# Kernel tuning notes

Hardware: AMD Instinct MI355X
Metric: run time of the kernel (lower is better)

## Reference

```python
import jax, jax.numpy as jnp
import numpy as np

B, N, K, H, NHEADS, NIN = 4, 2000, 30, 128, 4, 256
DFF = 4 * H
EPS = 1e-6


def layer_norm(x, gain, bias):
    # torch .var() defaults to unbiased (ddof=1); denominator is (sigma + eps)
    mu = x.mean(-1, keepdims=True)
    sigma = jnp.sqrt(x.var(-1, ddof=1, keepdims=True) + EPS)
    return gain * (x - mu) / (sigma + EPS) + bias


def setup_inputs() -> dict:
    key = jax.random.key(0)
    ks = jax.random.split(key, 10)
    s = 0.05
    h_v = jax.random.normal(ks[0], (B, N, H), jnp.float32)
    h_e = jax.random.normal(ks[1], (B, N, K, NIN), jnp.float32)
    mask_attend = (jax.random.uniform(ks[2], (B, N, K)) < 0.9).astype(jnp.float32)
    mask_attend = mask_attend.at[..., 0].set(1.0)  # avoid all-masked rows -> NaN softmax
    mask_v = (jax.random.uniform(ks[3], (B, N)) < 0.95).astype(jnp.float32)
    return {
        "h_v": h_v,
        "h_e": h_e,
        "mask_v": mask_v,
        "mask_attend": mask_attend,
        "W_Q": jax.random.normal(ks[4], (H, H), jnp.float32) * s,
        "W_K": jax.random.normal(ks[5], (H, NIN), jnp.float32) * s,
        "W_V": jax.random.normal(ks[6], (H, NIN), jnp.float32) * s,
        "W_O": jax.random.normal(ks[7], (H, H), jnp.float32) * s,
        "gain0": jnp.ones((H,), jnp.float32),
        "bias0": jnp.zeros((H,), jnp.float32),
        "gain1": jnp.ones((H,), jnp.float32),
        "bias1": jnp.zeros((H,), jnp.float32),
        "W_in": jax.random.normal(ks[8], (DFF, H), jnp.float32) * s,
        "b_in": jnp.zeros((DFF,), jnp.float32),
        "W_out": jax.random.normal(ks[9], (H, DFF), jnp.float32) * s,
        "b_out": jnp.zeros((H,), jnp.float32),
    }


def reference(h_v, h_e, mask_v, mask_attend, W_Q, W_K, W_V, W_O,
              gain0, bias0, gain1, bias1, W_in, b_in, W_out, b_out):
    d = H // NHEADS
    # Neighbor attention (dropout is identity at inference)
    Q = (h_v @ W_Q.T).reshape(B, N, NHEADS, d)          # [B,N,h,d]
    Kp = (h_e @ W_K.T).reshape(B, N, K, NHEADS, d)      # [B,N,K,h,d]
    Vp = (h_e @ W_V.T).reshape(B, N, K, NHEADS, d)      # [B,N,K,h,d]
    logits = jnp.einsum('bnhd,bnkhd->bnhk', Q, Kp) / np.sqrt(d)
    mask = mask_attend[:, :, None, :]                   # [B,N,1,K] broadcast over heads
    neg_inf = jnp.finfo(logits.dtype).min
    attend = jax.nn.softmax(jnp.where(mask > 0, logits, neg_inf), axis=-1) * mask
    h_upd = jnp.einsum('bnhk,bnkhd->bnhd', attend, Vp).reshape(B, N, H)
    dh = h_upd @ W_O.T
    h = layer_norm(h_v + dh, gain0, bias0)
    # Position-wise FFN
    dh = jax.nn.relu(h @ W_in.T + b_in) @ W_out.T + b_out
    h = layer_norm(h + dh, gain1, bias1)
    return mask_v[..., None] * h
```

## Files before the change

### kernel.cpp

```cpp
#include <hip/hip_runtime.h>
#include <math.h>

#define TK 30
#define TH 128
#define TNIN 256
#define TDFF 512
#define NTOK 8000
#define ROWP 264

typedef __attribute__((ext_vector_type(8))) short short8v;
typedef __attribute__((ext_vector_type(4))) short short4v;
typedef __attribute__((ext_vector_type(4))) float f32x4;

constexpr float LN_EPS = 1e-6f;
constexpr float NEG_INF = -3.402823466e38f;
constexpr float INV_SQRT_D = 0.17677669529663687f;

static __device__ __forceinline__ unsigned short f2bf(float f) {
  unsigned u = __float_as_uint(f);
  u = u + 0x7fffu + ((u >> 16) & 1u);
  return (unsigned short)(u >> 16);
}
static __device__ __forceinline__ float bf2f(unsigned short s) {
  return __uint_as_float(((unsigned)s) << 16);
}
static __device__ __forceinline__ void gload16(const void* gsrc, void* ldst) {
  __builtin_amdgcn_global_load_lds(
      (const __attribute__((address_space(1))) unsigned int*)gsrc,
      (__attribute__((address_space(3))) unsigned int*)ldst, 16, 0, 0);
}

__global__ void conv_weights_kernel(const float* __restrict__ W_K,
                                    const float* __restrict__ W_V,
                                    const float* __restrict__ W_Q,
                                    const float* __restrict__ W_O,
                                    const float* __restrict__ W_in,
                                    const float* __restrict__ W_out,
                                    unsigned short* __restrict__ Wc2,
                                    unsigned short* __restrict__ Wq2,
                                    unsigned short* __restrict__ Wp2,
                                    unsigned short* __restrict__ Wi2,
                                    unsigned short* __restrict__ Wo2)
{
  int idx = blockIdx.x * 256 + threadIdx.x;
  if (idx < 65536) {
    int e = idx >> 3, j = idx & 7;
    int kk = e >> 10, n = (e >> 6) & 15, lane = e & 63;
    int r = n*16 + (lane & 15);
    int c = kk*32 + (lane >> 4)*8 + j;
    float v = (r < TH) ? W_K[(size_t)r*TNIN + c] : W_V[(size_t)(r-TH)*TNIN + c];
    Wc2[idx] = f2bf(v);
  } else if (idx < 81920) {
    int i2 = idx - 65536;
    int e = i2 >> 3, j = i2 & 7;
    int kk = e >> 9, n = (e >> 6) & 7, lane = e & 63;
    int r = n*16 + (lane & 15);
    int c = kk*32 + (lane >> 4)*8 + j;
    Wq2[i2] = f2bf(W_Q[(size_t)r*TH + c]);
  } else if (idx < 98304) {
    int ip = idx - 81920;
    int e = ip >> 3, j = ip & 7;
    int kk = e >> 9, n = (e >> 6) & 7, lane = e & 63;
    int r = n*16 + (lane & 15);
    int c = kk*32 + (lane >> 4)*8 + j;
    Wp2[ip] = f2bf(W_O[(size_t)r*TH + c]);
  } else if (idx < 163840) {
    int i3 = idx - 98304;
    int e = i3 >> 3, j = i3 & 7;
    int ks = e >> 11, n = (e >> 6) & 31, lane = e & 63;
    int r = n*16 + (lane & 15);
    int c = ks*32 + (lane >> 4)*8 + j;
    Wi2[i3] = f2bf(W_in[(size_t)r*TH + c]);
  } else {
    int i4 = idx - 163840;
    int e = i4 >> 3, j = i4 & 7;
    int ks = e >> 9, n = (e >> 6) & 7, lane = e & 63;
    int r = n*16 + (lane & 15);
    int c = ks*32 + (lane >> 4)*8 + j;
    Wo2[i4] = f2bf(W_out[(size_t)r*TDFF + c]);
  }
}

__global__ __launch_bounds__(512, 4) void kvattn_kernel(
    const float* __restrict__ A, const unsigned short* __restrict__ Wc2,
    const unsigned short* __restrict__ Wq2, const float* __restrict__ h_v,
    const float* __restrict__ mask_attend, float* __restrict__ ul)
{
  const int tid  = threadIdx.x;
  const int wave = tid >> 6;
  const int lane = tid & 63;
  const int lm   = lane & 15;
  const int lgp  = lane >> 4;
  const int mh   = wave >> 2;
  const int nq   = wave & 3;
  const int bn0  = blockIdx.x * 4;

  __shared__ __align__(16) char smem[73728];
  unsigned short* Bl  = (unsigned short*)smem;
  unsigned short* Al  = (unsigned short*)(smem + 49152);
  unsigned short* KVs = (unsigned short*)smem;
  float* att = (float*)(smem + 67584);
  float* hvp = (float*)(smem + 69632);
  float* qvp = (float*)(smem + 71680);

  if (tid < 128) {
    int tok = tid >> 5, q = tid & 31;
    *(float4*)&hvp[tok*128 + q*4] = *(const float4*)&h_v[(size_t)(bn0 + tok)*TH + q*4];
  }

  const int rowa = tid >> 2, cga = tid & 3;
  const int rowc = (rowa > 119) ? 119 : rowa;
  const float* aptr = A + ((size_t)blockIdx.x*120 + rowc)*TNIN + cga*8;

  #define ISSUE_B(K)                                                             \
    { gload16(Wc2 + (size_t)(K)*8192 + tid*8,       &Bl[((K)%3)*8192 + tid*8]);  \
      gload16(Wc2 + (size_t)(K)*8192 + (tid+512)*8, &Bl[((K)%3)*8192 + (tid+512)*8]); }

  #define WRITE_A(K, S)                                                     \
    { short8v w;                                                            \
      w[0]=(short)f2bf(ra[S][0].x); w[1]=(short)f2bf(ra[S][0].y);           \
      w[2]=(short)f2bf(ra[S][0].z); w[3]=(short)f2bf(ra[S][0].w);           \
      w[4]=(short)f2bf(ra[S][1].x); w[5]=(short)f2bf(ra[S][1].y);           \
      w[6]=(short)f2bf(ra[S][1].z); w[7]=(short)f2bf(ra[S][1].w);           \
      *(short8v*)&Al[(((K)&1)*128 + rowa)*40 + cga*8] = w; }

  float4 ra[3][2];
  f32x4 acc[4][4] = {};

  ra[0][0] = *(const float4*)(aptr + 0);
  ra[0][1] = *(const float4*)(aptr + 4);
  ISSUE_B(0);
  ISSUE_B(1);
  ra[1][0] = *(const float4*)(aptr + 32);
  ra[1][1] = *(const float4*)(aptr + 36);
  ra[2][0] = *(const float4*)(aptr + 64);
  ra[2][1] = *(const float4*)(aptr + 68);
  WRITE_A(0, 0);

  #pragma unroll
  for (int k = 0; k < 8; ++k) {
    if (k == 7)      asm volatile("s_waitcnt vmcnt(0)" ::: "memory");
    else if (k == 6) asm volatile("s_waitcnt vmcnt(4)" ::: "memory");
    else             asm volatile("s_waitcnt vmcnt(6)" ::: "memory");
    __builtin_amdgcn_s_barrier();

    if (k < 6) ISSUE_B(k+2);
    if (k < 5) {
      ra[k%3][0] = *(const float4*)(aptr + (k+3)*32);
      ra[k%3][1] = *(const float4*)(aptr + (k+3)*32 + 4);
    }

    short8v af[4];
    #pragma unroll
    for (int m = 0; m < 4; ++m)
      af[m] = *(const short8v*)&Al[((k&1)*128 + mh*64 + m*16 + lm)*40 + lgp*8];

    __builtin_amdgcn_s_setprio(1);
    #pragma unroll
    for (int n = 0; n < 4; ++n) {
      short8v b = *(const short8v*)&Bl[(k%3)*8192 + ((nq*4 + n)*64 + lane)*8];
      #pragma unroll
      for (int m = 0; m < 4; ++m)
        acc[m][n] = __builtin_amdgcn_mfma_f32_16x16x32_bf16(b, af[m], acc[m][n], 0, 0, 0);
    }
    __builtin_amdgcn_s_setprio(0);

    if (k < 7) WRITE_A(k+1, (k+1)%3);
  }
  #undef ISSUE_B
  #undef WRITE_A

  __syncthreads();

  #pragma unroll
  for (int m = 0; m < 4; ++m) {
    int row = mh*64 + m*16 + lm;
    #pragma unroll
    for (int n = 0; n < 4; ++n) {
      int col = nq*64 + n*16 + lgp*4;
      short4v p;
      p[0]=(short)f2bf(acc[m][n][0]); p[1]=(short)f2bf(acc[m][n][1]);
      p[2]=(short)f2bf(acc[m][n][2]); p[3]=(short)f2bf(acc[m][n][3]);
      *(short4v*)&KVs[row*ROWP + col] = p;
    }
  }

  {
    f32x4 qacc = {};
    const int tokc = (lm < 4) ? lm : 3;
    #pragma unroll
    for (int ks = 0; ks < 4; ++ks) {
      short8v wq = *(const short8v*)(Wq2 + ((size_t)(ks*8 + wave)*64 + lane)*8);
      const float* hp = hvp + tokc*128 + ks*32 + lgp*8;
      float4 lo = *(const float4*)hp;
      float4 hi = *(const float4*)(hp + 4);
      short8v ha;
      ha[0]=(short)f2bf(lo.x); ha[1]=(short)f2bf(lo.y);
      ha[2]=(short)f2bf(lo.z); ha[3]=(short)f2bf(lo.w);
      ha[4]=(short)f2bf(hi.x); ha[5]=(short)f2bf(hi.y);
      ha[6]=(short)f2bf(hi.z); ha[7]=(short)f2bf(hi.w);
      qacc = __builtin_amdgcn_mfma_f32_16x16x32_bf16(wq, ha, qacc, 0, 0, 0);
    }
    if (lm < 4) *(f32x4*)&qvp[lm*128 + wave*16 + lgp*4] = qacc;
  }
  __syncthreads();

  {
    int tok = tid >> 7, h = (tid >> 5) & 3, k = tid & 31;
    int gtok = bn0 + tok;
    float s = 0.f;
    float ma = 0.f;
    if (k < TK) {
      const float* qp = &qvp[tok*128 + h*32];
      const unsigned short* kp = &KVs[(tok*TK + k)*ROWP + h*32];
      #pragma unroll
      for (int j = 0; j < 4; ++j) {
        short8v kf = *(const short8v*)(kp + j*8);
        float4 qa = *(const float4*)(qp + j*8);
        float4 qb = *(const float4*)(qp + j*8 + 4);
        s += qa.x*bf2f((unsigned short)kf[0]) + qa.y*bf2f((unsigned short)kf[1])
           + qa.z*bf2f((unsigned short)kf[2]) + qa.w*bf2f((unsigned short)kf[3])
           + qb.x*bf2f((unsigned short)kf[4]) + qb.y*bf2f((unsigned short)kf[5])
           + qb.z*bf2f((unsigned short)kf[6]) + qb.w*bf2f((unsigned short)kf[7]);
      }
      ma = mask_attend[(size_t)gtok*TK + k];
    }
    bool ok = (k < TK) && (ma > 0.f);
    float val = ok ? s * INV_SQRT_D : NEG_INF;
    float mm = val;
    #pragma unroll
    for (int d = 16; d >= 1; d >>= 1) mm = fmaxf(mm, __shfl_xor(mm, d, 32));
    float e = ok ? expf(val - mm) : 0.f;
    float ss = e;
    #pragma unroll
    for (int d = 16; d >= 1; d >>= 1) ss += __shfl_xor(ss, d, 32);
    att[(tok*4 + h)*32 + k] = e / ss;
  }
  __syncthreads();

  {
    int tok = tid >> 7, c = tid & 127;
    int gtok = bn0 + tok;
    const float* ar = &att[(tok*4 + (c >> 5))*32];
    const unsigned short* vb = &KVs[tok*TK*ROWP + TH + c];
    float u = 0.f;
    #pragma unroll
    for (int k = 0; k < TK; ++k)
      u += ar[k] * bf2f(vb[k*ROWP]);
    ul[(size_t)gtok*TH + c] = u;
  }
}

__global__ __launch_bounds__(256) void ffn_all_kernel(
    const float* __restrict__ ul, const unsigned short* __restrict__ Wp2,
    const float* __restrict__ h_v,
    const float* __restrict__ gain0, const float* __restrict__ bias0,
    const unsigned short* __restrict__ Wi2, const unsigned short* __restrict__ Wo2,
    const float* __restrict__ b_in, const float* __restrict__ b_out,
    const float* __restrict__ gain1, const float* __restrict__ bias1,
    const float* __restrict__ mask_v, float* __restrict__ out)
{
  const int tid  = threadIdx.x;
  const int tok0 = blockIdx.x * 32;
  const int wave = tid >> 6;
  const int lane = tid & 63;
  const int lm   = lane & 15;
  const int lgp  = lane >> 4;

  __shared__ __align__(16) char smem[143616];
  unsigned short* Wp  = (unsigned short*)smem;
  unsigned short* Wst = (unsigned short*)(smem + 32768);
  unsigned short* At  = (unsigned short*)(smem + 98304);
  unsigned short* Zs  = (unsigned short*)(smem + 107008);
  float* bin  = (float*)(smem + 140288);
  float* part = (float*)(smem + 142336);
  float* red  = (float*)(smem + 143360);

  for (int t = tid; t < 1024; t += 256) {
    int row = t >> 5, q = t & 31;
    float4 v = *(const float4*)&ul[(size_t)(tok0+row)*TH + q*4];
    short4v w;
    w[0]=(short)f2bf(v.x); w[1]=(short)f2bf(v.y);
    w[2]=(short)f2bf(v.z); w[3]=(short)f2bf(v.w);
    *(short4v*)&At[row*136 + q*4] = w;
  }
  if (tid < 128) *(float4*)&bin[tid*4] = *(const float4*)&b_in[tid*4];
  #pragma unroll
  for (int p = 0; p < 8; ++p)
    gload16(Wp2 + (size_t)(tid + p*256)*8, &Wp[(tid + p*256)*8]);
  #pragma unroll
  for (int p = 0; p < 8; ++p)
    gload16(Wi2 + (size_t)(tid + p*256)*8, &Wst[(tid + p*256)*8]);

  asm volatile("s_waitcnt vmcnt(8)" ::: "memory");
  __syncthreads();

  f32x4 acco[2][2] = {};
  #pragma unroll
  for (int ks = 0; ks < 4; ++ks) {
    short8v a0 = *(const short8v*)&At[lm*136      + ks*32 + lgp*8];
    short8v a1 = *(const short8v*)&At[(16+lm)*136 + ks*32 + lgp*8];
    #pragma unroll
    for (int n = 0; n < 2; ++n) {
      short8v b = *(const short8v*)&Wp[((size_t)(ks*8 + wave*2 + n)*64 + lane)*8];
      acco[0][n] = __builtin_amdgcn_mfma_f32_16x16x32_bf16(b, a0, acco[0][n], 0, 0, 0);
      acco[1][n] = __builtin_amdgcn_mfma_f32_16x16x32_bf16(b, a1, acco[1][n], 0, 0, 0);
    }
  }

  f32x4 hn[2][2];
  {
    f32x4 x[2][2];
    float s1r[2] = {0.f, 0.f}, s2r[2] = {0.f, 0.f};
    #pragma unroll
    for (int m = 0; m < 2; ++m) {
      int row = m*16 + lm;
      #pragma unroll
      for (int n = 0; n < 2; ++n) {
        int col = (wave*2 + n)*16 + lgp*4;
        float4 hv = *(const float4*)&h_v[(size_t)(tok0+row)*TH + col];
        x[m][n][0] = acco[m][n][0] + hv.x;
        x[m][n][1] = acco[m][n][1] + hv.y;
        x[m][n][2] = acco[m][n][2] + hv.z;
        x[m][n][3] = acco[m][n][3] + hv.w;
        #pragma unroll
        for (int r = 0; r < 4; ++r) {
          s1r[m] += x[m][n][r];
          s2r[m] += x[m][n][r]*x[m][n][r];
        }
      }
    }
    #pragma unroll
    for (int m = 0; m < 2; ++m) {
      s1r[m] += __shfl_xor(s1r[m], 16); s2r[m] += __shfl_xor(s2r[m], 16);
      s1r[m] += __shfl_xor(s1r[m], 32); s2r[m] += __shfl_xor(s2r[m], 32);
    }
    if (lgp == 0) {
      part[(lm*4      + wave)*2 + 0] = s1r[0];
      part[(lm*4      + wave)*2 + 1] = s2r[0];
      part[((16+lm)*4 + wave)*2 + 0] = s1r[1];
      part[((16+lm)*4 + wave)*2 + 1] = s2r[1];
    }
    __syncthreads();
    if (tid < 32) {
      float s1 = 0.f, s2 = 0.f;
      #pragma unroll
      for (int w = 0; w < 4; ++w) { s1 += part[(tid*4+w)*2]; s2 += part[(tid*4+w)*2+1]; }
      float mu  = s1*(1.f/128.f);
      float var = (s2 - 128.f*mu*mu)*(1.f/127.f);
      red[tid*2]   = mu;
      red[tid*2+1] = 1.f/(sqrtf(var+LN_EPS)+LN_EPS);
    }
    __syncthreads();
    #pragma unroll
    for (int m = 0; m < 2; ++m) {
      int row = m*16 + lm;
      float mu = red[row*2], inv = red[row*2+1];
      #pragma unroll
      for (int n = 0; n < 2; ++n) {
        int col = (wave*2 + n)*16 + lgp*4;
        float4 g = *(const float4*)&gain0[col];
        float4 b = *(const float4*)&bias0[col];
        hn[m][n][0] = g.x*(x[m][n][0]-mu)*inv + b.x;
        hn[m][n][1] = g.y*(x[m][n][1]-mu)*inv + b.y;
        hn[m][n][2] = g.z*(x[m][n][2]-mu)*inv + b.z;
        hn[m][n][3] = g.w*(x[m][n][3]-mu)*inv + b.w;
        short4v p;
        p[0]=(short)f2bf(hn[m][n][0]); p[1]=(short)f2bf(hn[m][n][1]);
        p[2]=(short)f2bf(hn[m][n][2]); p[3]=(short)f2bf(hn[m][n][3]);
        *(short4v*)&At[row*136 + col] = p;
      }
    }
  }

  f32x4 acc1[2][8] = {};
  #pragma unroll
  for (int ks = 0; ks < 4; ++ks) {
    asm volatile("s_waitcnt vmcnt(0)" ::: "memory");
    __builtin_amdgcn_s_barrier();
    if (ks < 3) {
      #pragma unroll
      for (int p = 0; p < 8; ++p)
        gload16(Wi2 + (size_t)(ks+1)*16384 + (tid + p*256)*8,
                &Wst[((ks+1)&1)*16384 + (tid + p*256)*8]);
    } else {
      #pragma unroll
      for (int p = 0; p < 4; ++p)
        gload16(Wo2 + (size_t)(tid + p*256)*8, &Wst[(tid + p*256)*8]);
    }

    short8v a0 = *(const short8v*)&At[lm*136      + ks*32 + lgp*8];
    short8v a1 = *(const short8v*)&At[(16+lm)*136 + ks*32 + lgp*8];
    #pragma unroll
    for (int n = 0; n < 8; ++n) {
      short8v b = *(const short8v*)&Wst[(ks&1)*16384 + ((wave*8 + n)*64 + lane)*8];
      acc1[0][n] = __builtin_amdgcn_mfma_f32_16x16x32_bf16(b, a0, acc1[0][n], 0, 0, 0);
      acc1[1][n] = __builtin_amdgcn_mfma_f32_16x16x32_bf16(b, a1, acc1[1][n], 0, 0, 0);
    }
  }

  #pragma unroll
  for (int m = 0; m < 2; ++m) {
    int row = m*16 + lm;
    #pragma unroll
    for (int n = 0; n < 8; ++n) {
      int col = (wave*8 + n)*16 + lgp*4;
      float4 bv = *(const float4*)&bin[col];
      short4v p;
      p[0]=(short)f2bf(fmaxf(acc1[m][n][0] + bv.x, 0.f));
      p[1]=(short)f2bf(fmaxf(acc1[m][n][1] + bv.y, 0.f));
      p[2]=(short)f2bf(fmaxf(acc1[m][n][2] + bv.z, 0.f));
      p[3]=(short)f2bf(fmaxf(acc1[m][n][3] + bv.w, 0.f));
      *(short4v*)&Zs[row*520 + col] = p;
    }
  }

  f32x4 acc2[2][2] = {};
  #pragma unroll
  for (int ks2 = 0; ks2 < 8; ++ks2) {
    asm volatile("s_waitcnt vmcnt(0)" ::: "memory");
    __builtin_amdgcn_s_barrier();
    if (ks2 < 7) {
      #pragma unroll
      for (int p = 0; p < 4; ++p)
        gload16(Wo2 + (size_t)(ks2+1)*8192 + (tid + p*256)*8,
                &Wst[((ks2+1)&1)*8192 + (tid + p*256)*8]);
    }

    #pragma unroll
    for (int s = 0; s < 2; ++s) {
      int ks = ks2*2 + s;
      short8v a0 = *(const short8v*)&Zs[lm*520      + ks*32 + lgp*8];
      short8v a1 = *(const short8v*)&Zs[(16+lm)*520 + ks*32 + lgp*8];
      #pragma unroll
      for (int n = 0; n < 2; ++n) {
        short8v b = *(const short8v*)&Wst[(ks2&1)*8192 + s*4096 + ((wave*2 + n)*64 + lane)*8];
        acc2[0][n] = __builtin_amdgcn_mfma_f32_16x16x32_bf16(b, a0, acc2[0][n], 0, 0, 0);
        acc2[1][n] = __builtin_amdgcn_mfma_f32_16x16x32_bf16(b, a1, acc2[1][n], 0, 0, 0);
      }
    }
  }

  {
    f32x4 x[2][2];
    float s1r[2] = {0.f, 0.f}, s2r[2] = {0.f, 0.f};
    #pragma unroll
    for (int m = 0; m < 2; ++m) {
      #pragma unroll
      for (int n = 0; n < 2; ++n) {
        int col = (wave*2 + n)*16 + lgp*4;
        float4 bo = *(const float4*)&b_out[col];
        x[m][n][0] = acc2[m][n][0] + bo.x + hn[m][n][0];
        x[m][n][1] = acc2[m][n][1] + bo.y + hn[m][n][1];
        x[m][n][2] = acc2[m][n][2] + bo.z + hn[m][n][2];
        x[m][n][3] = acc2[m][n][3] + bo.w + hn[m][n][3];
        #pragma unroll
        for (int r = 0; r < 4; ++r) {
          s1r[m] += x[m][n][r];
          s2r[m] += x[m][n][r]*x[m][n][r];
        }
      }
    }
    #pragma unroll
    for (int m = 0; m < 2; ++m) {
      s1r[m] += __shfl_xor(s1r[m], 16); s2r[m] += __shfl_xor(s2r[m], 16);
      s1r[m] += __shfl_xor(s1r[m], 32); s2r[m] += __shfl_xor(s2r[m], 32);
    }
    if (lgp == 0) {
      part[(lm*4      + wave)*2 + 0] = s1r[0];
      part[(lm*4      + wave)*2 + 1] = s2r[0];
      part[((16+lm)*4 + wave)*2 + 0] = s1r[1];
      part[((16+lm)*4 + wave)*2 + 1] = s2r[1];
    }
    __syncthreads();
    if (tid < 32) {
      float s1 = 0.f, s2 = 0.f;
      #pragma unroll
      for (int w = 0; w < 4; ++w) { s1 += part[(tid*4+w)*2]; s2 += part[(tid*4+w)*2+1]; }
      float mu  = s1*(1.f/128.f);
      float var = (s2 - 128.f*mu*mu)*(1.f/127.f);
      red[tid*2]   = mu;
      red[tid*2+1] = 1.f/(sqrtf(var+LN_EPS)+LN_EPS);
    }
    __syncthreads();
    #pragma unroll
    for (int m = 0; m < 2; ++m) {
      int row = m*16 + lm;
      float mu = red[row*2], inv = red[row*2+1];
      float mv = mask_v[tok0 + row];
      #pragma unroll
      for (int n = 0; n < 2; ++n) {
        int col = (wave*2 + n)*16 + lgp*4;
        float4 g = *(const float4*)&gain1[col];
        float4 b = *(const float4*)&bias1[col];
        float4 y;
        y.x = mv*(g.x*(x[m][n][0]-mu)*inv + b.x);
        y.y = mv*(g.y*(x[m][n][1]-mu)*inv + b.y);
        y.z = mv*(g.z*(x[m][n][2]-mu)*inv + b.z);
        y.w = mv*(g.w*(x[m][n][3]-mu)*inv + b.w);
        *(float4*)&out[(size_t)(tok0+row)*TH + col] = y;
      }
    }
  }
}

extern "C" void kernel_launch(void* const* d_in, const int* in_sizes, int n_in,
                              void* d_out, int out_size, void* d_ws, size_t ws_size,
                              hipStream_t stream)
{
  const float* h_v         = (const float*)d_in[0];
  const float* h_e         = (const float*)d_in[1];
  const float* mask_v      = (const float*)d_in[2];
  const float* mask_attend = (const float*)d_in[3];
  const float* W_Q   = (const float*)d_in[4];
  const float* W_K   = (const float*)d_in[5];
  const float* W_V   = (const float*)d_in[6];
  const float* W_O   = (const float*)d_in[7];
  const float* gain0 = (const float*)d_in[8];
  const float* bias0 = (const float*)d_in[9];
  const float* gain1 = (const float*)d_in[10];
  const float* bias1 = (const float*)d_in[11];
  const float* W_in  = (const float*)d_in[12];
  const float* b_in  = (const float*)d_in[13];
  const float* W_out = (const float*)d_in[14];
  const float* b_out = (const float*)d_in[15];

  float* out = (float*)d_out;
  char* ws = (char*)d_ws;
  unsigned short* Wc2 = (unsigned short*)ws;
  unsigned short* Wq2 = (unsigned short*)(ws + 131072);
  unsigned short* Wp2 = (unsigned short*)(ws + 163840);
  unsigned short* Wi2 = (unsigned short*)(ws + 196608);
  unsigned short* Wo2 = (unsigned short*)(ws + 327680);
  float* ul = (float*)(ws + 458752);

  conv_weights_kernel<<<896, 256, 0, stream>>>(W_K, W_V, W_Q, W_O, W_in, W_out,
                                               Wc2, Wq2, Wp2, Wi2, Wo2);
  kvattn_kernel<<<NTOK/4, 512, 0, stream>>>(h_e, Wc2, Wq2, h_v, mask_attend, ul);
  ffn_all_kernel<<<NTOK/32, 256, 0, stream>>>(ul, Wp2, h_v, gain0, bias0,
                                              Wi2, Wo2, b_in, b_out,
                                              gain1, bias1, mask_v, out);
}
```

Baseline: 79.89 us.

## Halve kvattn block to 256 threads with each wave covering all 128 rows

The fused K/V projection and attention kernel now runs with 4 waves per block instead of 8. Each wave computes all 128 A-rows (8 M-fragments) for its 64-column slice, so the B operand is reused across twice as many MFMAs and waves no longer split rows. Global loads, the Q projection, and the softmax and value passes are redistributed across the smaller block, with two passes where needed. The cost is more accumulator registers per thread (32 f32x4) and half the threads for latency hiding. Shared memory stays at 73728 bytes per block, which may limit how many blocks fit per CU.

```diff
diff --git a/kernel.cpp b/kernel.cpp
--- a/kernel.cpp
+++ b/kernel.cpp
@@ -81,18 +81,16 @@
   }
 }
 
-__global__ __launch_bounds__(512, 4) void kvattn_kernel(
+__global__ __launch_bounds__(256, 2) void kvattn_kernel(
     const float* __restrict__ A, const unsigned short* __restrict__ Wc2,
     const unsigned short* __restrict__ Wq2, const float* __restrict__ h_v,
     const float* __restrict__ mask_attend, float* __restrict__ ul)
 {
   const int tid  = threadIdx.x;
-  const int wave = tid >> 6;
+  const int nq   = tid >> 6;
   const int lane = tid & 63;
   const int lm   = lane & 15;
   const int lgp  = lane >> 4;
-  const int mh   = wave >> 2;
-  const int nq   = wave & 3;
   const int bn0  = blockIdx.x * 4;
 
   __shared__ __align__(16) char smem[73728];
@@ -108,59 +106,67 @@
     *(float4*)&hvp[tok*128 + q*4] = *(const float4*)&h_v[(size_t)(bn0 + tok)*TH + q*4];
   }
 
-  const int rowa = tid >> 2, cga = tid & 3;
+  const int rowa = tid >> 1, ha = tid & 1;
   const int rowc = (rowa > 119) ? 119 : rowa;
-  const float* aptr = A + ((size_t)blockIdx.x*120 + rowc)*TNIN + cga*8;
-
-  #define ISSUE_B(K)                                                             \
-    { gload16(Wc2 + (size_t)(K)*8192 + tid*8,       &Bl[((K)%3)*8192 + tid*8]);  \
-      gload16(Wc2 + (size_t)(K)*8192 + (tid+512)*8, &Bl[((K)%3)*8192 + (tid+512)*8]); }
+  const float* aptr = A + ((size_t)blockIdx.x*120 + rowc)*TNIN + ha*16;
+
+  #define ISSUE_B(K)                                                               \
+    { gload16(Wc2 + (size_t)(K)*8192 + (tid      )*8, &Bl[((K)%3)*8192 + (tid      )*8]); \
+      gload16(Wc2 + (size_t)(K)*8192 + (tid+ 256 )*8, &Bl[((K)%3)*8192 + (tid+ 256 )*8]); \
+      gload16(Wc2 + (size_t)(K)*8192 + (tid+ 512 )*8, &Bl[((K)%3)*8192 + (tid+ 512 )*8]); \
+      gload16(Wc2 + (size_t)(K)*8192 + (tid+ 768 )*8, &Bl[((K)%3)*8192 + (tid+ 768 )*8]); }
+
+  #define LOAD_RA(S, K)                                                     \
+    { ra[S][0] = *(const float4*)(aptr + (K)*32);                           \
+      ra[S][1] = *(const float4*)(aptr + (K)*32 + 4);                       \
+      ra[S][2] = *(const float4*)(aptr + (K)*32 + 8);                       \
+      ra[S][3] = *(const float4*)(aptr + (K)*32 + 12); }
 
   #define WRITE_A(K, S)                                                     \
-    { short8v w;                                                            \
-      w[0]=(short)f2bf(ra[S][0].x); w[1]=(short)f2bf(ra[S][0].y);           \
-      w[2]=(short)f2bf(ra[S][0].z); w[3]=(short)f2bf(ra[S][0].w);           \
-      w[4]=(short)f2bf(ra[S][1].x); w[5]=(short)f2bf(ra[S][1].y);           \
-      w[6]=(short)f2bf(ra[S][1].z); w[7]=(short)f2bf(ra[S][1].w);           \
-      *(short8v*)&Al[(((K)&1)*128 + rowa)*40 + cga*8] = w; }
-
-  float4 ra[3][2];
-  f32x4 acc[4][4] = {};
-
-  ra[0][0] = *(const float4*)(aptr + 0);
-  ra[0][1] = *(const float4*)(aptr + 4);
+    { short8v w0, w1;                                                       \
+      w0[0]=(short)f2bf(ra[S][0].x); w0[1]=(short)f2bf(ra[S][0].y);         \
+      w0[2]=(short)f2bf(ra[S][0].z); w0[3]=(short)f2bf(ra[S][0].w);         \
+      w0[4]=(short)f2bf(ra[S][1].x); w0[5]=(short)f2bf(ra[S][1].y);         \
+      w0[6]=(short)f2bf(ra[S][1].z); w0[7]=(short)f2bf(ra[S][1].w);         \
+      w1[0]=(short)f2bf(ra[S][2].x); w1[1]=(short)f2bf(ra[S][2].y);         \
+      w1[2]=(short)f2bf(ra[S][2].z); w1[3]=(short)f2bf(ra[S][2].w);         \
+      w1[4]=(short)f2bf(ra[S][3].x); w1[5]=(short)f2bf(ra[S][3].y);         \
+      w1[6]=(short)f2bf(ra[S][3].z); w1[7]=(short)f2bf(ra[S][3].w);         \
+      *(short8v*)&Al[(((K)&1)*128 + rowa)*40 + ha*16    ] = w0;             \
+      *(short8v*)&Al[(((K)&1)*128 + rowa)*40 + ha*16 + 8] = w1; }
+
+  float4 ra[3][4];
+  f32x4 acc[8][4] = {};
+
+  LOAD_RA(0, 0);
   ISSUE_B(0);
   ISSUE_B(1);
-  ra[1][0] = *(const float4*)(aptr + 32);
-  ra[1][1] = *(const float4*)(aptr + 36);
-  ra[2][0] = *(const float4*)(aptr + 64);
-  ra[2][1] = *(const float4*)(aptr + 68);
+  LOAD_RA(1, 1);
+  LOAD_RA(2, 2);
   WRITE_A(0, 0);
 
   #pragma unroll
   for (int k = 0; k < 8; ++k) {
-    if (k == 7)      asm volatile("s_waitcnt vmcnt(0)" ::: "memory");
-    else if (k == 6) asm volatile("s_waitcnt vmcnt(4)" ::: "memory");
-    else             asm volatile("s_waitcnt vmcnt(6)" ::: "memory");
+    if      (k == 0) asm volatile("s_waitcnt vmcnt(8)"  ::: "memory");
+    else if (k <= 5) asm volatile("s_waitcnt vmcnt(12)" ::: "memory");
+    else if (k == 6) asm volatile("s_waitcnt vmcnt(8)"  ::: "memory");
+    else             asm volatile("s_waitcnt vmcnt(0)"  ::: "memory");
     __builtin_amdgcn_s_barrier();
 
     if (k < 6) ISSUE_B(k+2);
-    if (k < 5) {
-      ra[k%3][0] = *(const float4*)(aptr + (k+3)*32);
-      ra[k%3][1] = *(const float4*)(aptr + (k+3)*32 + 4);
-    }
-
-    short8v af[4];
-    #pragma unroll
-    for (int m = 0; m < 4; ++m)
-      af[m] = *(const short8v*)&Al[((k&1)*128 + mh*64 + m*16 + lm)*40 + lgp*8];
+    if (k < 5) LOAD_RA(k%3, k+3);
+
+    short8v af[8];
+    #pragma unroll
+    for (int m = 0; m < 8; ++m)
+      af[m] = *(const short8v*)&Al[((k&1)*128 + m*16 + lm)*40 + lgp*8];
 
     __builtin_amdgcn_s_setprio(1);
     #pragma unroll
     for (int n = 0; n < 4; ++n) {
       short8v b = *(const short8v*)&Bl[(k%3)*8192 + ((nq*4 + n)*64 + lane)*8];
       #pragma unroll
-      for (int m = 0; m < 4; ++m)
+      for (int m = 0; m < 8; ++m)
         acc[m][n] = __builtin_amdgcn_mfma_f32_16x16x32_bf16(b, af[m], acc[m][n], 0, 0, 0);
     }
     __builtin_amdgcn_s_setprio(0);
@@ -168,16 +174,17 @@
     if (k < 7) WRITE_A(k+1, (k+1)%3);
   }
   #undef ISSUE_B
+  #undef LOAD_RA
   #undef WRITE_A
 
   __syncthreads();
 
   #pragma unroll
-  for (int m = 0; m < 4; ++m) {
-    int row = mh*64 + m*16 + lm;
+  for (int m = 0; m < 8; ++m) {
+    int row = m*16 + lm;
     #pragma unroll
     for (int n = 0; n < 4; ++n) {
-      int col = nq*64 + n*16 + lgp*4;
+      int col = (nq*4 + n)*16 + lgp*4;
       short4v p;
       p[0]=(short)f2bf(acc[m][n][0]); p[1]=(short)f2bf(acc[m][n][1]);
       p[2]=(short)f2bf(acc[m][n][2]); p[3]=(short)f2bf(acc[m][n][3]);
@@ -186,27 +193,31 @@
   }
 
   {
-    f32x4 qacc = {};
     const int tokc = (lm < 4) ? lm : 3;
     #pragma unroll
-    for (int ks = 0; ks < 4; ++ks) {
-      short8v wq = *(const short8v*)(Wq2 + ((size_t)(ks*8 + wave)*64 + lane)*8);
-      const float* hp = hvp + tokc*128 + ks*32 + lgp*8;
-      float4 lo = *(const float4*)hp;
-      float4 hi = *(const float4*)(hp + 4);
-      short8v ha;
-      ha[0]=(short)f2bf(lo.x); ha[1]=(short)f2bf(lo.y);
-      ha[2]=(short)f2bf(lo.z); ha[3]=(short)f2bf(lo.w);
-      ha[4]=(short)f2bf(hi.x); ha[5]=(short)f2bf(hi.y);
-      ha[6]=(short)f2bf(hi.z); ha[7]=(short)f2bf(hi.w);
-      qacc = __builtin_amdgcn_mfma_f32_16x16x32_bf16(wq, ha, qacc, 0, 0, 0);
-    }
-    if (lm < 4) *(f32x4*)&qvp[lm*128 + wave*16 + lgp*4] = qacc;
+    for (int nf = 0; nf < 2; ++nf) {
+      f32x4 qacc = {};
+      #pragma unroll
+      for (int ks = 0; ks < 4; ++ks) {
+        short8v wq = *(const short8v*)(Wq2 + ((size_t)(ks*8 + nq*2 + nf)*64 + lane)*8);
+        const float* hp = hvp + tokc*128 + ks*32 + lgp*8;
+        float4 lo = *(const float4*)hp;
+        float4 hi = *(const float4*)(hp + 4);
+        short8v ha_;
+        ha_[0]=(short)f2bf(lo.x); ha_[1]=(short)f2bf(lo.y);
+        ha_[2]=(short)f2bf(lo.z); ha_[3]=(short)f2bf(lo.w);
+        ha_[4]=(short)f2bf(hi.x); ha_[5]=(short)f2bf(hi.y);
+        ha_[6]=(short)f2bf(hi.z); ha_[7]=(short)f2bf(hi.w);
+        qacc = __builtin_amdgcn_mfma_f32_16x16x32_bf16(wq, ha_, qacc, 0, 0, 0);
+      }
+      if (lm < 4) *(f32x4*)&qvp[lm*128 + (nq*2 + nf)*16 + lgp*4] = qacc;
+    }
   }
   __syncthreads();
 
-  {
-    int tok = tid >> 7, h = (tid >> 5) & 3, k = tid & 31;
+  #pragma unroll
+  for (int pass = 0; pass < 2; ++pass) {
+    int tok = (tid >> 7) + 2*pass, h = (tid >> 5) & 3, k = tid & 31;
     int gtok = bn0 + tok;
     float s = 0.f;
     float ma = 0.f;
@@ -238,8 +249,9 @@
   }
   __syncthreads();
 
-  {
-    int tok = tid >> 7, c = tid & 127;
+  #pragma unroll
+  for (int pass = 0; pass < 2; ++pass) {
+    int tok = (tid >> 7) + 2*pass, c = tid & 127;
     int gtok = bn0 + tok;
     const float* ar = &att[(tok*4 + (c >> 5))*32];
     const unsigned short* vb = &KVs[tok*TK*ROWP + TH + c];
@@ -536,7 +548,7 @@
 
   conv_weights_kernel<<<896, 256, 0, stream>>>(W_K, W_V, W_Q, W_O, W_in, W_out,
                                                Wc2, Wq2, Wp2, Wi2, Wo2);
-  kvattn_kernel<<<NTOK/4, 512, 0, stream>>>(h_e, Wc2, Wq2, h_v, mask_attend, ul);
+  kvattn_kernel<<<NTOK/4, 256, 0, stream>>>(h_e, Wc2, Wq2, h_v, mask_attend, ul);
   ffn_all_kernel<<<NTOK/32, 256, 0, stream>>>(ul, Wp2, h_v, gain0, bias0,
                                               Wi2, Wo2, b_in, b_out,
                                               gain1, bias1, mask_v, out);
```

Result: slower. 92.97 us (+16.4%).

## Halve tokens per block in KV-attention kernel and double-buffer weight tiles

Applied to the files above, without the earlier changes.

The KV/attention kernel now handles 2 tokens (60 edge rows) per block instead of 4 (120 rows), and launches twice as many blocks. The weight-tile ring buffer in shared memory shrinks from triple to double buffering, and each thread now loads one float4 of edge features per k-step instead of two. Together these cut LDS use from about 72 KB to 45 KB and raise launch bounds to 6 blocks per CU, aiming for more resident waves to hide latency on the memory-bound h_e stream. The trade-off is that each projection-weight tile is fetched twice as often in total, the MFMA tile per wave is smaller, half the threads sit idle in the softmax and V phases, and prefetch depth is shallower.

```diff
diff --git a/kernel.cpp b/kernel.cpp
--- a/kernel.cpp
+++ b/kernel.cpp
@@ -81,7 +81,7 @@
   }
 }
 
-__global__ __launch_bounds__(512, 4) void kvattn_kernel(
+__global__ __launch_bounds__(512, 6) void kvattn_kernel(
     const float* __restrict__ A, const unsigned short* __restrict__ Wc2,
     const unsigned short* __restrict__ Wq2, const float* __restrict__ h_v,
     const float* __restrict__ mask_attend, float* __restrict__ ul)
@@ -93,74 +93,67 @@
   const int lgp  = lane >> 4;
   const int mh   = wave >> 2;
   const int nq   = wave & 3;
-  const int bn0  = blockIdx.x * 4;
-
-  __shared__ __align__(16) char smem[73728];
+  const int bn0  = blockIdx.x * 2;
+
+  __shared__ __align__(16) char smem[46080];
   unsigned short* Bl  = (unsigned short*)smem;
-  unsigned short* Al  = (unsigned short*)(smem + 49152);
+  unsigned short* Al  = (unsigned short*)(smem + 32768);
   unsigned short* KVs = (unsigned short*)smem;
-  float* att = (float*)(smem + 67584);
-  float* hvp = (float*)(smem + 69632);
-  float* qvp = (float*)(smem + 71680);
-
-  if (tid < 128) {
+  float* hvp = (float*)(smem + 43008);
+  float* qvp = (float*)(smem + 44032);
+  float* att = (float*)(smem + 45056);
+
+  if (tid < 64) {
     int tok = tid >> 5, q = tid & 31;
     *(float4*)&hvp[tok*128 + q*4] = *(const float4*)&h_v[(size_t)(bn0 + tok)*TH + q*4];
   }
 
-  const int rowa = tid >> 2, cga = tid & 3;
-  const int rowc = (rowa > 119) ? 119 : rowa;
-  const float* aptr = A + ((size_t)blockIdx.x*120 + rowc)*TNIN + cga*8;
-
-  #define ISSUE_B(K)                                                             \
-    { gload16(Wc2 + (size_t)(K)*8192 + tid*8,       &Bl[((K)%3)*8192 + tid*8]);  \
-      gload16(Wc2 + (size_t)(K)*8192 + (tid+512)*8, &Bl[((K)%3)*8192 + (tid+512)*8]); }
+  const int rowa = tid >> 3, cga = tid & 7;
+  const int rowc = (rowa > 59) ? 59 : rowa;
+  const float* aptr = A + ((size_t)blockIdx.x*60 + rowc)*TNIN + cga*4;
+
+  #define ISSUE_B(K)                                                               \
+    { gload16(Wc2 + (size_t)(K)*8192 + tid*8,       &Bl[((K)&1)*8192 + tid*8]);    \
+      gload16(Wc2 + (size_t)(K)*8192 + (tid+512)*8, &Bl[((K)&1)*8192 + (tid+512)*8]); }
+
+  #define LOAD_RA(S, K)  { ra[S] = *(const float4*)(aptr + (K)*32); }
 
   #define WRITE_A(K, S)                                                     \
-    { short8v w;                                                            \
-      w[0]=(short)f2bf(ra[S][0].x); w[1]=(short)f2bf(ra[S][0].y);           \
-      w[2]=(short)f2bf(ra[S][0].z); w[3]=(short)f2bf(ra[S][0].w);           \
-      w[4]=(short)f2bf(ra[S][1].x); w[5]=(short)f2bf(ra[S][1].y);           \
-      w[6]=(short)f2bf(ra[S][1].z); w[7]=(short)f2bf(ra[S][1].w);           \
-      *(short8v*)&Al[(((K)&1)*128 + rowa)*40 + cga*8] = w; }
-
-  float4 ra[3][2];
-  f32x4 acc[4][4] = {};
-
-  ra[0][0] = *(const float4*)(aptr + 0);
-  ra[0][1] = *(const float4*)(aptr + 4);
+    { short4v w;                                                            \
+      w[0]=(short)f2bf(ra[S].x); w[1]=(short)f2bf(ra[S].y);                 \
+      w[2]=(short)f2bf(ra[S].z); w[3]=(short)f2bf(ra[S].w);                 \
+      *(short4v*)&Al[(((K)&1)*64 + rowa)*40 + cga*4] = w; }
+
+  float4 ra[3];
+  f32x4 acc[2][4] = {};
+
+  LOAD_RA(0, 0);
   ISSUE_B(0);
-  ISSUE_B(1);
-  ra[1][0] = *(const float4*)(aptr + 32);
-  ra[1][1] = *(const float4*)(aptr + 36);
-  ra[2][0] = *(const float4*)(aptr + 64);
-  ra[2][1] = *(const float4*)(aptr + 68);
+  LOAD_RA(1, 1);
+  LOAD_RA(2, 2);
   WRITE_A(0, 0);
 
   #pragma unroll
   for (int k = 0; k < 8; ++k) {
-    if (k == 7)      asm volatile("s_waitcnt vmcnt(0)" ::: "memory");
-    else if (k == 6) asm volatile("s_waitcnt vmcnt(4)" ::: "memory");
-    else             asm volatile("s_waitcnt vmcnt(6)" ::: "memory");
+    if      (k <= 5) asm volatile("s_waitcnt vmcnt(2)" ::: "memory");
+    else if (k == 6) asm volatile("s_waitcnt vmcnt(1)" ::: "memory");
+    else             asm volatile("s_waitcnt vmcnt(0)" ::: "memory");
     __builtin_amdgcn_s_barrier();
 
-    if (k < 6) ISSUE_B(k+2);
-    if (k < 5) {
-      ra[k%3][0] = *(const float4*)(aptr + (k+3)*32);
-      ra[k%3][1] = *(const float4*)(aptr + (k+3)*32 + 4);
-    }
-
-    short8v af[4];
-    #pragma unroll
-    for (int m = 0; m < 4; ++m)
-      af[m] = *(const short8v*)&Al[((k&1)*128 + mh*64 + m*16 + lm)*40 + lgp*8];
+    if (k < 7) ISSUE_B(k+1);
+    if (k < 5) LOAD_RA(k%3, k+3);
+
+    short8v af[2];
+    #pragma unroll
+    for (int m = 0; m < 2; ++m)
+      af[m] = *(const short8v*)&Al[((k&1)*64 + mh*32 + m*16 + lm)*40 + lgp*8];
 
     __builtin_amdgcn_s_setprio(1);
     #pragma unroll
     for (int n = 0; n < 4; ++n) {
-      short8v b = *(const short8v*)&Bl[(k%3)*8192 + ((nq*4 + n)*64 + lane)*8];
-      #pragma unroll
-      for (int m = 0; m < 4; ++m)
+      short8v b = *(const short8v*)&Bl[(k&1)*8192 + ((nq*4 + n)*64 + lane)*8];
+      #pragma unroll
+      for (int m = 0; m < 2; ++m)
         acc[m][n] = __builtin_amdgcn_mfma_f32_16x16x32_bf16(b, af[m], acc[m][n], 0, 0, 0);
     }
     __builtin_amdgcn_s_setprio(0);
@@ -168,13 +161,14 @@
     if (k < 7) WRITE_A(k+1, (k+1)%3);
   }
   #undef ISSUE_B
+  #undef LOAD_RA
   #undef WRITE_A
 
   __syncthreads();
 
   #pragma unroll
-  for (int m = 0; m < 4; ++m) {
-    int row = mh*64 + m*16 + lm;
+  for (int m = 0; m < 2; ++m) {
+    int row = mh*32 + m*16 + lm;
     #pragma unroll
     for (int n = 0; n < 4; ++n) {
       int col = nq*64 + n*16 + lgp*4;
@@ -187,7 +181,7 @@
 
   {
     f32x4 qacc = {};
-    const int tokc = (lm < 4) ? lm : 3;
+    const int tokc = (lm < 2) ? lm : 1;
     #pragma unroll
     for (int ks = 0; ks < 4; ++ks) {
       short8v wq = *(const short8v*)(Wq2 + ((size_t)(ks*8 + wave)*64 + lane)*8);
@@ -201,11 +195,11 @@
       ha[6]=(short)f2bf(hi.z); ha[7]=(short)f2bf(hi.w);
       qacc = __builtin_amdgcn_mfma_f32_16x16x32_bf16(wq, ha, qacc, 0, 0, 0);
     }
-    if (lm < 4) *(f32x4*)&qvp[lm*128 + wave*16 + lgp*4] = qacc;
+    if (lm < 2) *(f32x4*)&qvp[lm*128 + wave*16 + lgp*4] = qacc;
   }
   __syncthreads();
 
-  {
+  if (tid < 256) {
     int tok = tid >> 7, h = (tid >> 5) & 3, k = tid & 31;
     int gtok = bn0 + tok;
     float s = 0.f;
@@ -238,11 +232,11 @@
   }
   __syncthreads();
 
-  {
+  if (tid < 256) {
     int tok = tid >> 7, c = tid & 127;
     int gtok = bn0 + tok;
     const float* ar = &att[(tok*4 + (c >> 5))*32];
-    const unsigned short* vb = &KVs[tok*TK*ROWP + TH + c];
+    const unsigned short* vb = &KVs[(tok*TK)*ROWP + TH + c];
     float u = 0.f;
     #pragma unroll
     for (int k = 0; k < TK; ++k)
@@ -536,7 +530,7 @@
 
   conv_weights_kernel<<<896, 256, 0, stream>>>(W_K, W_V, W_Q, W_O, W_in, W_out,
                                                Wc2, Wq2, Wp2, Wi2, Wo2);
-  kvattn_kernel<<<NTOK/4, 512, 0, stream>>>(h_e, Wc2, Wq2, h_v, mask_attend, ul);
+  kvattn_kernel<<<NTOK/2, 512, 0, stream>>>(h_e, Wc2, Wq2, h_v, mask_attend, ul);
   ffn_all_kernel<<<NTOK/32, 256, 0, stream>>>(ul, Wp2, h_v, gain0, bias0,
                                               Wi2, Wo2, b_in, b_out,
                                               gain1, bias1, mask_v, out);
```

Result: slower. 88.60 us (+10.9%).

## Stage full A tile in LDS once and stream B weights directly from global

Applied to the files above, without the earlier changes.

Replaces the triple-buffered LDS pipeline for the K/V projection GEMM with a simpler scheme. The whole 128x256 A tile is converted to bf16 and staged in LDS up front behind a single barrier. Each wave then loads its B fragments straight from global memory into registers, double-buffered across k-steps, which removes the per-iteration barriers and the B staging through LDS. The cost is that global loads of A no longer overlap with the MFMAs, each wave fetches B from global or cache on its own instead of sharing it, and register pressure rises.

```diff
diff --git a/kernel.cpp b/kernel.cpp
--- a/kernel.cpp
+++ b/kernel.cpp
@@ -96,92 +96,53 @@
   const int bn0  = blockIdx.x * 4;
 
   __shared__ __align__(16) char smem[73728];
-  unsigned short* Bl  = (unsigned short*)smem;
-  unsigned short* Al  = (unsigned short*)(smem + 49152);
+  unsigned short* Ab  = (unsigned short*)smem;
   unsigned short* KVs = (unsigned short*)smem;
-  float* att = (float*)(smem + 67584);
-  float* hvp = (float*)(smem + 69632);
-  float* qvp = (float*)(smem + 71680);
+  float* hvp = (float*)(smem + 67584);
+  float* qvp = (float*)(smem + 69632);
+  float* att = (float*)(smem + 71680);
 
   if (tid < 128) {
     int tok = tid >> 5, q = tid & 31;
     *(float4*)&hvp[tok*128 + q*4] = *(const float4*)&h_v[(size_t)(bn0 + tok)*TH + q*4];
   }
 
-  const int rowa = tid >> 2, cga = tid & 3;
-  const int rowc = (rowa > 119) ? 119 : rowa;
-  const float* aptr = A + ((size_t)blockIdx.x*120 + rowc)*TNIN + cga*8;
-
-  #define ISSUE_B(K)                                                             \
-    { gload16(Wc2 + (size_t)(K)*8192 + tid*8,       &Bl[((K)%3)*8192 + tid*8]);  \
-      gload16(Wc2 + (size_t)(K)*8192 + (tid+512)*8, &Bl[((K)%3)*8192 + (tid+512)*8]); }
-
-  #define WRITE_A(K, S)                                                     \
-    { short8v w;                                                            \
-      w[0]=(short)f2bf(ra[S][0].x); w[1]=(short)f2bf(ra[S][0].y);           \
-      w[2]=(short)f2bf(ra[S][0].z); w[3]=(short)f2bf(ra[S][0].w);           \
-      w[4]=(short)f2bf(ra[S][1].x); w[5]=(short)f2bf(ra[S][1].y);           \
-      w[6]=(short)f2bf(ra[S][1].z); w[7]=(short)f2bf(ra[S][1].w);           \
-      *(short8v*)&Al[(((K)&1)*128 + rowa)*40 + cga*8] = w; }
-
-  float4 ra[3][2];
+  #pragma unroll
+  for (int i = 0; i < 16; ++i) {
+    int idx = tid + i*512;
+    int row = idx >> 6, cg = idx & 63;
+    int rowc = (row > 119) ? 119 : row;
+    float4 v = *(const float4*)&A[((size_t)blockIdx.x*120 + rowc)*TNIN + cg*4];
+    short4v w;
+    w[0]=(short)f2bf(v.x); w[1]=(short)f2bf(v.y);
+    w[2]=(short)f2bf(v.z); w[3]=(short)f2bf(v.w);
+    *(short4v*)&Ab[row*ROWP + cg*4] = w;
+  }
+  __syncthreads();
+
   f32x4 acc[4][4] = {};
-
-  ra[0][0] = *(const float4*)(aptr + 0);
-  ra[0][1] = *(const float4*)(aptr + 4);
-  ISSUE_B(0);
-  ISSUE_B(1);
-  ra[1][0] = *(const float4*)(aptr + 32);
-  ra[1][1] = *(const float4*)(aptr + 36);
-  ra[2][0] = *(const float4*)(aptr + 64);
-  ra[2][1] = *(const float4*)(aptr + 68);
-  WRITE_A(0, 0);
+  short8v bcur[4], bnxt[4];
+  #pragma unroll
+  for (int n = 0; n < 4; ++n)
+    bcur[n] = *(const short8v*)(Wc2 + ((size_t)(nq*4 + n)*64 + lane)*8);
 
   #pragma unroll
   for (int k = 0; k < 8; ++k) {
-    if (k == 7)      asm volatile("s_waitcnt vmcnt(0)" ::: "memory");
-    else if (k == 6) asm volatile("s_waitcnt vmcnt(4)" ::: "memory");
-    else             asm volatile("s_waitcnt vmcnt(6)" ::: "memory");
-    __builtin_amdgcn_s_barrier();
-
-    if (k < 6) ISSUE_B(k+2);
-    if (k < 5) {
-      ra[k%3][0] = *(const float4*)(aptr + (k+3)*32);
-      ra[k%3][1] = *(const float4*)(aptr + (k+3)*32 + 4);
-    }
-
-    short8v af[4];
-    #pragma unroll
-    for (int m = 0; m < 4; ++m)
-      af[m] = *(const short8v*)&Al[((k&1)*128 + mh*64 + m*16 + lm)*40 + lgp*8];
-
-    __builtin_amdgcn_s_setprio(1);
-    #pragma unroll
-    for (int n = 0; n < 4; ++n) {
-      short8v b = *(const short8v*)&Bl[(k%3)*8192 + ((nq*4 + n)*64 + lane)*8];
-      #pragma unroll
-      for (int m = 0; m < 4; ++m)
-        acc[m][n] = __builtin_amdgcn_mfma_f32_16x16x32_bf16(b, af[m], acc[m][n], 0, 0, 0);
-    }
-    __builtin_amdgcn_s_setprio(0);
-
-    if (k < 7) WRITE_A(k+1, (k+1)%3);
-  }
-  #undef ISSUE_B
-  #undef WRITE_A
-
-  __syncthreads();
-
-  #pragma unroll
-  for (int m = 0; m < 4; ++m) {
-    int row = mh*64 + m*16 + lm;
-    #pragma unroll
-    for (int n = 0; n < 4; ++n) {
-      int col = nq*64 + n*16 + lgp*4;
-      short4v p;
-      p[0]=(short)f2bf(acc[m][n][0]); p[1]=(short)f2bf(acc[m][n][1]);
-      p[2]=(short)f2bf(acc[m][n][2]); p[3]=(short)f2bf(acc[m][n][3]);
-      *(short4v*)&KVs[row*ROWP + col] = p;
+    if (k < 7) {
+      #pragma unroll
+      for (int n = 0; n < 4; ++n)
+        bnxt[n] = *(const short8v*)(Wc2 + ((size_t)((k+1)*16 + nq*4 + n)*64 + lane)*8);
+    }
+    #pragma unroll
+    for (int m = 0; m < 4; ++m) {
+      short8v a = *(const short8v*)&Ab[(mh*64 + m*16 + lm)*ROWP + k*32 + lgp*8];
+      #pragma unroll
+      for (int n = 0; n < 4; ++n)
+        acc[m][n] = __builtin_amdgcn_mfma_f32_16x16x32_bf16(bcur[n], a, acc[m][n], 0, 0, 0);
+    }
+    if (k < 7) {
+      #pragma unroll
+      for (int n = 0; n < 4; ++n) bcur[n] = bnxt[n];
     }
   }
 
@@ -202,6 +163,21 @@
       qacc = __builtin_amdgcn_mfma_f32_16x16x32_bf16(wq, ha, qacc, 0, 0, 0);
     }
     if (lm < 4) *(f32x4*)&qvp[lm*128 + wave*16 + lgp*4] = qacc;
+  }
+
+  __syncthreads();
+
+  #pragma unroll
+  for (int m = 0; m < 4; ++m) {
+    int row = mh*64 + m*16 + lm;
+    #pragma unroll
+    for (int n = 0; n < 4; ++n) {
+      int col = nq*64 + n*16 + lgp*4;
+      short4v p;
+      p[0]=(short)f2bf(acc[m][n][0]); p[1]=(short)f2bf(acc[m][n][1]);
+      p[2]=(short)f2bf(acc[m][n][2]); p[3]=(short)f2bf(acc[m][n][3]);
+      *(short4v*)&KVs[row*ROWP + col] = p;
+    }
   }
   __syncthreads();
 
```

After: 85.83 us. +7.4%, slower.
